# Kernel tuning notes

Measured on AMD Instinct MI355X. Metric: run time of the kernel, lower is better.

The kernel has to match this reference:

```python
import jax, jax.numpy as jnp
import numpy as np

D_MODEL = 1024
NHEAD = 16
DHEAD = D_MODEL // NHEAD
DFF = 4096
B, S = 2, 2048
R = 25                # local_attention_radius = 5*5
K = 5                 # rel_pos_max_distance
W = 2 * R + 1         # window width
EPS = 1e-5


def setup_inputs() -> dict:
    key = jax.random.key(0)
    ks = jax.random.split(key, 12)
    s = 0.02
    g = lambda k, shape: jax.random.normal(k, shape, jnp.float32) * s
    return {
        "src": jax.random.normal(ks[0], (B, S, D_MODEL), jnp.float32),
        # attention in/out projections (W stored [out,in], applied x @ W.T + b)
        "wq": g(ks[1], (D_MODEL, D_MODEL)), "bq": jnp.zeros((D_MODEL,), jnp.float32),
        "wk": g(ks[2], (D_MODEL, D_MODEL)), "bk": jnp.zeros((D_MODEL,), jnp.float32),
        "wv": g(ks[3], (D_MODEL, D_MODEL)), "bv": jnp.zeros((D_MODEL,), jnp.float32),
        "wo": g(ks[4], (D_MODEL, D_MODEL)), "bo": jnp.zeros((D_MODEL,), jnp.float32),
        # relative position embeddings, ids clipped to [-K, K] -> 2K+1 rows
        "rel_emb": g(ks[5], (2 * K + 1, DHEAD)),
        # FFN
        "w1": g(ks[6], (DFF, D_MODEL)), "b1": jnp.zeros((DFF,), jnp.float32),
        "w2": g(ks[7], (D_MODEL, DFF)), "b2": jnp.zeros((D_MODEL,), jnp.float32),
        # layernorms
        "g1": jnp.ones((D_MODEL,), jnp.float32), "beta1": jnp.zeros((D_MODEL,), jnp.float32),
        "g2": jnp.ones((D_MODEL,), jnp.float32), "beta2": jnp.zeros((D_MODEL,), jnp.float32),
    }


def _layernorm(x, g, b):
    m = x.mean(-1, keepdims=True)
    v = ((x - m) ** 2).mean(-1, keepdims=True)
    return (x - m) * jax.lax.rsqrt(v + EPS) * g + b


def _rel_window_attention(x, wq, bq, wk, bk, wv, bv, wo, bo, rel_emb):
    b, s, d = x.shape

    def proj(w, bias):
        return (x @ w.T + bias).reshape(b, s, NHEAD, DHEAD).transpose(0, 2, 1, 3)

    q = proj(wq, bq)  # [B,H,S,Dh]
    k = proj(wk, bk)
    v = proj(wv, bv)

    offsets = jnp.arange(-R, R + 1)                     # [W]
    j = jnp.arange(s)[:, None] + offsets[None, :]       # [S,W] absolute key index
    valid = (j >= 0) & (j < s)
    jc = jnp.clip(j, 0, s - 1)

    scale = 1.0 / np.sqrt(DHEAD).astype(np.float32)
    k_win = k[:, :, jc]                                 # [B,H,S,W,Dh] banded gather
    scores = jnp.einsum('bhsd,bhswd->bhsw', q, k_win) * scale
    rel_ids = jnp.clip(offsets, -K, K) + K              # [W]
    scores = scores + jnp.einsum('bhsd,wd->bhsw', q, rel_emb[rel_ids]) * scale
    scores = jnp.where(valid[None, None], scores, jnp.float32(-1e30))
    attn = jax.nn.softmax(scores, axis=-1)              # [B,H,S,W]

    v_win = v[:, :, jc]                                 # [B,H,S,W,Dh]
    out = jnp.einsum('bhsw,bhswd->bhsd', attn, v_win)
    out = out.transpose(0, 2, 1, 3).reshape(b, s, d)
    return out @ wo.T + bo


def reference(src, wq, bq, wk, bk, wv, bv, wo, bo, rel_emb,
              w1, b1, w2, b2, g1, beta1, g2, beta2):
    # post-norm (norm_first=False default) transformer block, dropout=0 (eval)
    z = _rel_window_attention(src, wq, bq, wk, bk, wv, bv, wo, bo, rel_emb)
    x = _layernorm(src + z, g1, beta1)
    ff = jax.nn.relu(x @ w1.T + b1) @ w2.T + b2
    return _layernorm(x + ff, g2, beta2)
```

## Files before the change

### kernel.cpp

```cpp
#include <hip/hip_runtime.h>


#define D_MODEL 1024
#define SEQ     2048
#define NROWS   4096
#define WIN     51
#define RAD     25

typedef __attribute__((ext_vector_type(8))) __bf16 bf16x8;
typedef __attribute__((ext_vector_type(4))) float  floatx4;

__device__ __forceinline__ unsigned short f2bf(float x) {
    unsigned u = __float_as_uint(x);
    unsigned r = u + 0x7fffu + ((u >> 16) & 1u);
    return (unsigned short)(r >> 16);
}
__device__ __forceinline__ float bf2f(unsigned short h) {
    return __uint_as_float(((unsigned)h) << 16);
}

__device__ __forceinline__ void gld16(const unsigned short* g, unsigned short* l) {
    __builtin_amdgcn_global_load_lds(
        (const __attribute__((address_space(1))) unsigned int*)g,
        (__attribute__((address_space(3))) unsigned int*)l,
        16, 0, 0);
}

__device__ __forceinline__ void cvtgrp(const float* __restrict__ in,
                                       unsigned short* __restrict__ out, int g) {
    float4 f = ((const float4*)in)[g];
    ushort4 u;
    u.x = f2bf(f.x); u.y = f2bf(f.y); u.z = f2bf(f.z); u.w = f2bf(f.w);
    ((ushort4*)out)[g] = u;
}

__global__ __launch_bounds__(256)
void cvt_all(const float* __restrict__ src,
             const float* __restrict__ wq, const float* __restrict__ wk,
             const float* __restrict__ wv, const float* __restrict__ wo,
             const float* __restrict__ w1, const float* __restrict__ w2,
             const float* __restrict__ bq, const float* __restrict__ bk,
             const float* __restrict__ bv,
             unsigned short* __restrict__ xb,
             unsigned short* __restrict__ wqkvb,
             unsigned short* __restrict__ wob,
             unsigned short* __restrict__ w1b,
             unsigned short* __restrict__ w2b,
             float* __restrict__ bqkv)
{
    int g = blockIdx.x * 256 + threadIdx.x;
    if (g >= 4194496) return;
    if (g < 1048576) { cvtgrp(src, xb, g); return; }
    g -= 1048576;
    if (g < 262144) { cvtgrp(wq, wqkvb, g); return; }
    g -= 262144;
    if (g < 262144) { cvtgrp(wk, wqkvb + 1048576, g); return; }
    g -= 262144;
    if (g < 262144) { cvtgrp(wv, wqkvb + 2097152, g); return; }
    g -= 262144;
    if (g < 262144) { cvtgrp(wo, wob, g); return; }
    g -= 262144;
    if (g < 1048576) { cvtgrp(w1, w1b, g); return; }
    g -= 1048576;
    if (g < 1048576) { cvtgrp(w2, w2b, g); return; }
    g -= 1048576;
    float4 f = (g < 64) ? ((const float4*)bq)[g]
             : (g < 128) ? ((const float4*)bk)[g - 64]
                         : ((const float4*)bv)[g - 128];
    ((float4*)bqkv)[g] = f;
}

__global__ __launch_bounds__(256, 2)
void gemm_dp(const unsigned short* __restrict__ A,
             const unsigned short* __restrict__ Wt,
             const float* __restrict__ bias,
             unsigned short* __restrict__ Cb,
             int kstride, int kloop, int T, int tncnt,
             int ldc, int relu, size_t sstep1, size_t sstep2)
{
    __shared__ __attribute__((aligned(16))) unsigned short AS[3 * 8192];
    __shared__ __attribute__((aligned(16))) unsigned short BS[3 * 4096];

    const int id = blockIdx.x;
    const int s  = id / T;
    const int t0 = id - s * T;
    const int sid = (t0 & 7) * (T >> 3) + (t0 >> 3);
    const int bm = (sid / tncnt) * 256;
    const int bn = (sid % tncnt) * 128;

    const int tid  = threadIdx.x;
    const int lane = tid & 63;
    const int wave = tid >> 6;
    const int wr   = wave >> 1;
    const int wc   = wave & 1;
    const int fm   = lane & 15;
    const int fq   = lane >> 4;

    const int kofs = s * kloop;
    const int NT   = kloop >> 5;

    const int ks  = (tid >> 3) & 7;
    const int gi  = tid ^ ks;
    const int r0s = gi >> 2;
    const int c2s = gi & 3;
    const unsigned short* Agp = A  + (size_t)(bm + r0s) * kstride + kofs + c2s * 8;
    const unsigned short* Wgp = Wt + (size_t)(bn + r0s) * kstride + kofs + c2s * 8;
    const size_t istep = (size_t)64 * kstride;

    const int rA  = wr * 128 + fm;
    const int rB  = wc * 64  + fm;
    const int c0A = ((((rA << 2) | fq) ^ (fm >> 1)) << 3);
    const int c0B = ((((rB << 2) | fq) ^ (fm >> 1)) << 3);

    {
        const unsigned short* Ap = Agp;
        const unsigned short* Wp = Wgp;
        gld16(Ap,             AS + tid * 8);
        gld16(Ap + istep,     AS + tid * 8 + 2048);
        gld16(Ap + 2 * istep, AS + tid * 8 + 4096);
        gld16(Ap + 3 * istep, AS + tid * 8 + 6144);
        gld16(Wp,             BS + tid * 8);
        gld16(Wp + istep,     BS + tid * 8 + 2048);
        Ap += 32; Wp += 32;
        gld16(Ap,             AS + 8192 + tid * 8);
        gld16(Ap + istep,     AS + 8192 + tid * 8 + 2048);
        gld16(Ap + 2 * istep, AS + 8192 + tid * 8 + 4096);
        gld16(Ap + 3 * istep, AS + 8192 + tid * 8 + 6144);
        gld16(Wp,             BS + 4096 + tid * 8);
        gld16(Wp + istep,     BS + 4096 + tid * 8 + 2048);
    }
    asm volatile("s_waitcnt vmcnt(6)" ::: "memory");
    __builtin_amdgcn_sched_barrier(0);
    __builtin_amdgcn_s_barrier();
    __builtin_amdgcn_sched_barrier(0);

    floatx4 acc[8][4] = {};
    const unsigned short* Aga = Agp + 64;
    const unsigned short* Wga = Wgp + 64;
    int cbA = 0, cbB = 0;
    int pbA = 16384, pbB = 8192;

    for (int t = 0; t < NT; t++) {
        const bool pf = (t + 2 < NT);

        bf16x8 af[8], bf[4];
        #pragma unroll
        for (int mi = 0; mi < 8; mi++)
            af[mi] = *(const bf16x8*)(AS + cbA + c0A + mi * 512);
        #pragma unroll
        for (int ni = 0; ni < 4; ni++)
            bf[ni] = *(const bf16x8*)(BS + cbB + c0B + ni * 512);

        if (pf) {
            gld16(Aga,             AS + pbA + tid * 8);
            gld16(Aga + istep,     AS + pbA + tid * 8 + 2048);
            gld16(Aga + 2 * istep, AS + pbA + tid * 8 + 4096);
            gld16(Aga + 3 * istep, AS + pbA + tid * 8 + 6144);
            gld16(Wga,             BS + pbB + tid * 8);
            gld16(Wga + istep,     BS + pbB + tid * 8 + 2048);
        }

        __builtin_amdgcn_s_setprio(1);
        #pragma unroll
        for (int mi = 0; mi < 8; mi++)
            #pragma unroll
            for (int ni = 0; ni < 4; ni++)
                acc[mi][ni] = __builtin_amdgcn_mfma_f32_16x16x32_bf16(
                    af[mi], bf[ni], acc[mi][ni], 0, 0, 0);
        __builtin_amdgcn_s_setprio(0);

        if (t + 1 < NT) {
            if (pf) asm volatile("s_waitcnt vmcnt(6)" ::: "memory");
            else    asm volatile("s_waitcnt vmcnt(0)" ::: "memory");
            __builtin_amdgcn_sched_barrier(0);
            __builtin_amdgcn_s_barrier();
            __builtin_amdgcn_sched_barrier(0);
        }
        cbA = (cbA == 16384) ? 0 : cbA + 8192;
        cbB = (cbB == 8192)  ? 0 : cbB + 4096;
        pbA = (pbA == 16384) ? 0 : pbA + 8192;
        pbB = (pbB == 8192)  ? 0 : pbB + 4096;
        Aga += 32;
        Wga += 32;
    }

    unsigned short* Co = Cb + (size_t)(s & 1) * sstep1 + (size_t)(s >> 1) * sstep2;
    const int r0  = bm + wr * 128 + fq * 4;
    const int c0e = bn + wc * 64 + fm;
    #pragma unroll
    for (int mi = 0; mi < 8; mi++) {
        #pragma unroll
        for (int ni = 0; ni < 4; ni++) {
            const int col = c0e + ni * 16;
            const float bv = bias ? bias[col] : 0.0f;
            #pragma unroll
            for (int rr = 0; rr < 4; rr++) {
                const int row = r0 + mi * 16 + rr;
                float v = acc[mi][ni][rr] + bv;
                if (relu) v = fmaxf(v, 0.0f);
                Co[(size_t)row * ldc + col] = f2bf(v);
            }
        }
    }
}

__global__ __launch_bounds__(512, 2)
void gemm8p(const unsigned short* __restrict__ A,
            const unsigned short* __restrict__ Wt,
            const float* __restrict__ bias,
            unsigned short* __restrict__ Cb,
            int kstride, int kloop, int T, int tncnt,
            int ldc, int relu, size_t sstep1, size_t sstep2)
{
    __shared__ __attribute__((aligned(16))) unsigned short AS[2 * 16384];
    __shared__ __attribute__((aligned(16))) unsigned short BS[2 * 16384];

    const int id = blockIdx.x;
    const int sl = id / T;
    const int t0 = id - sl * T;
    const int sid = (t0 & 7) * (T >> 3) + (t0 >> 3);
    const int bm = (sid / tncnt) * 256;
    const int bn = (sid % tncnt) * 256;

    const int tid  = threadIdx.x;
    const int lane = tid & 63;
    const int wave = tid >> 6;
    const int wr   = wave >> 2;
    const int wc   = wave & 3;
    const int fm   = lane & 15;
    const int fq   = lane >> 4;

    const int kofs  = sl * kloop;
    const int NITER = kloop >> 7;

    const int srow = tid >> 3;
    const int scol = ((tid & 7) ^ ((tid >> 3) & 7)) * 8;
    const unsigned short* PA = A  + (size_t)(bm + srow) * kstride + kofs + scol;
    const unsigned short* PW = Wt + (size_t)(bn + srow) * kstride + kofs + scol;
    const size_t rs64 = (size_t)64 * kstride;

    const int aoff = (wr * 128 + fm) * 64;
    const int boff = (wc * 64  + fm) * 64;
    const int ck0  = (fq ^ (fm & 7)) * 8;
    const int ck1  = ck0 ^ 32;

    floatx4 acc[8][4] = {};

    auto STG = [&](const unsigned short* g, int h, unsigned short* l) {
        gld16(g + (size_t)(2 * h)     * rs64, l + h * 8192 + tid * 8);
        gld16(g + (size_t)(2 * h + 1) * rs64, l + h * 8192 + 4096 + tid * 8);
    };
    auto rdA = [&](bf16x8 (&d)[4][2], int bufb, int mb) {
        #pragma unroll
        for (int mi = 0; mi < 4; mi++) {
            d[mi][0] = *(const bf16x8*)(AS + bufb + aoff + (mb + mi) * 1024 + ck0);
            d[mi][1] = *(const bf16x8*)(AS + bufb + aoff + (mb + mi) * 1024 + ck1);
        }
    };
    auto rdB = [&](bf16x8 (&d)[2][2], int bufb, int nb) {
        #pragma unroll
        for (int ni = 0; ni < 2; ni++) {
            d[ni][0] = *(const bf16x8*)(BS + bufb + boff + (nb + ni) * 1024 + ck0);
            d[ni][1] = *(const bf16x8*)(BS + bufb + boff + (nb + ni) * 1024 + ck1);
        }
    };
    auto mmq = [&](bf16x8 (&a)[4][2], bf16x8 (&b)[2][2], int mb, int nb) {
        __builtin_amdgcn_s_setprio(1);
        #pragma unroll
        for (int ks = 0; ks < 2; ks++)
            #pragma unroll
            for (int mi = 0; mi < 4; mi++)
                #pragma unroll
                for (int ni = 0; ni < 2; ni++)
                    acc[mb + mi][nb + ni] = __builtin_amdgcn_mfma_f32_16x16x32_bf16(
                        a[mi][ks], b[ni][ks], acc[mb + mi][nb + ni], 0, 0, 0);
        __builtin_amdgcn_s_setprio(0);
    };
    auto barpre = [&]() {
        __builtin_amdgcn_sched_barrier(0);
        __builtin_amdgcn_s_barrier();
        asm volatile("s_waitcnt lgkmcnt(0)" ::: "memory");
        __builtin_amdgcn_sched_barrier(0);
    };
    auto barpost = [&]() {
        __builtin_amdgcn_sched_barrier(0);
        __builtin_amdgcn_s_barrier();
        __builtin_amdgcn_sched_barrier(0);
    };

    unsigned short* AS0 = AS;            unsigned short* AS1 = AS + 16384;
    unsigned short* BS0 = BS;            unsigned short* BS1 = BS + 16384;

    STG(PA, 0, AS0); STG(PA, 1, AS0);
    STG(PW, 0, BS0); STG(PW, 1, BS0);
    STG(PW + 64, 0, BS1); STG(PW + 64, 1, BS1);
    __builtin_amdgcn_sched_barrier(0);
    asm volatile("s_waitcnt vmcnt(4)" ::: "memory");
    __builtin_amdgcn_sched_barrier(0);
    __builtin_amdgcn_s_barrier();
    __builtin_amdgcn_sched_barrier(0);

    for (int it = 0; it < NITER; it++) {
        const bool more = (it + 1 < NITER);
        bf16x8 a03[4][2], a47[4][2], b01[2][2], b23[2][2];

        rdA(a03, 0, 0); rdB(b01, 0, 0);
        STG(PA + 64, 0, AS1);
        barpre(); mmq(a03, b01, 0, 0); barpost();
        rdB(b23, 0, 2);
        STG(PA + 64, 1, AS1);
        barpre(); mmq(a03, b23, 0, 2); barpost();
        rdA(a47, 0, 4);
        if (more) STG(PW + 128, 0, BS0);
        barpre(); mmq(a47, b01, 4, 0); barpost();
        if (more) STG(PW + 128, 1, BS0);
        __builtin_amdgcn_sched_barrier(0);
        if (more) asm volatile("s_waitcnt vmcnt(4)" ::: "memory");
        else      asm volatile("s_waitcnt vmcnt(0)" ::: "memory");
        __builtin_amdgcn_sched_barrier(0);
        __builtin_amdgcn_s_barrier();
        __builtin_amdgcn_sched_barrier(0);
        mmq(a47, b23, 4, 2); barpost();
        rdA(a03, 16384, 0); rdB(b01, 16384, 0);
        if (more) STG(PA + 128, 0, AS0);
        barpre(); mmq(a03, b01, 0, 0); barpost();
        rdB(b23, 16384, 2);
        if (more) STG(PA + 128, 1, AS0);
        barpre(); mmq(a03, b23, 0, 2); barpost();
        rdA(a47, 16384, 4);
        if (more) STG(PW + 192, 0, BS1);
        barpre(); mmq(a47, b01, 4, 0); barpost();
        if (more) {
            STG(PW + 192, 1, BS1);
            __builtin_amdgcn_sched_barrier(0);
            asm volatile("s_waitcnt vmcnt(4)" ::: "memory");
        }
        __builtin_amdgcn_sched_barrier(0);
        __builtin_amdgcn_s_barrier();
        __builtin_amdgcn_sched_barrier(0);
        mmq(a47, b23, 4, 2); barpost();

        PA += 128; PW += 128;
    }

    unsigned short* Co = Cb + (size_t)(sl & 1) * sstep1 + (size_t)(sl >> 1) * sstep2;
    const int r0  = bm + wr * 128 + fq * 4;
    const int c0e = bn + wc * 64 + fm;
    #pragma unroll
    for (int mi = 0; mi < 8; mi++) {
        #pragma unroll
        for (int ni = 0; ni < 4; ni++) {
            const int col = c0e + ni * 16;
            const float bv = bias ? bias[col] : 0.0f;
            #pragma unroll
            for (int rr = 0; rr < 4; rr++) {
                const int row = r0 + mi * 16 + rr;
                float v = acc[mi][ni][rr] + bv;
                if (relu) v = fmaxf(v, 0.0f);
                Co[(size_t)row * ldc + col] = f2bf(v);
            }
        }
    }
}

__global__ __launch_bounds__(256, 2)
void attn_mfma(const unsigned short* __restrict__ qkv,
               const float* __restrict__ rel,
               unsigned short* __restrict__ attnb)
{
    __shared__ __attribute__((aligned(16))) unsigned short Qs[64 * 72];
    __shared__ __attribute__((aligned(16))) unsigned short Ks[128 * 72];
    __shared__ __attribute__((aligned(16))) unsigned short Vt[64 * 168];
    __shared__ __attribute__((aligned(16))) unsigned short Rs[16 * 72];
    __shared__ __attribute__((aligned(16))) unsigned short Pl[4 * 16 * 104];
    __shared__ float Qrl[4 * 16 * 12];

    const int t   = threadIdx.x;
    const int blk = blockIdx.x;
    const int st  = blk & 31;
    const int h   = (blk >> 5) & 15;
    const int b   = blk >> 9;
    const int s0  = st << 6;
    const int brow0 = b * SEQ;

    const int trow = t >> 3;
    const int tc   = (t & 7) * 8;
    const uint4 z4 = make_uint4(0, 0, 0, 0);

    #pragma unroll
    for (int p = 0; p < 2; p++) {
        int r = trow + p * 32;
        uint4 v = *(const uint4*)(qkv + (size_t)(brow0 + s0 + r) * 3072 + h * 64 + tc);
        *(uint4*)(Qs + r * 72 + tc) = v;
    }
    #pragma unroll
    for (int p = 0; p < 4; p++) {
        int kr = trow + p * 32;
        int ka = s0 - 25 + kr;
        bool in = (ka >= 0) & (ka < SEQ);
        uint4 kv = z4, vv = z4;
        if (in) {
            kv = *(const uint4*)(qkv + (size_t)(brow0 + ka) * 3072 + 1024 + h * 64 + tc);
            vv = *(const uint4*)(qkv + (size_t)(brow0 + ka) * 3072 + 2048 + h * 64 + tc);
        }
        *(uint4*)(Ks + kr * 72 + tc) = kv;
        const unsigned short* e = (const unsigned short*)&vv;
        #pragma unroll
        for (int j = 0; j < 8; j++)
            Vt[(tc + j) * 168 + kr] = e[j];
    }
    if (t < 176) {
        float4 f = ((const float4*)rel)[t];
        int fi = t * 4, rr = fi >> 6, cc = fi & 63;
        ushort4 u;
        u.x = f2bf(f.x); u.y = f2bf(f.y); u.z = f2bf(f.z); u.w = f2bf(f.w);
        *(ushort4*)(Rs + rr * 72 + cc) = u;
    } else {
        int fi = 704 + (t - 176) * 4, rr = fi >> 6, cc = fi & 63;
        *(ushort4*)(Rs + rr * 72 + cc) = make_ushort4(0, 0, 0, 0);
    }
    {
        int n = t * 4, w2 = n >> 8, rem = n & 255, rr = rem >> 4, cc = 80 + (rem & 15);
        *(ushort4*)(Pl + w2 * (16 * 104) + rr * 104 + cc) = make_ushort4(0, 0, 0, 0);
    }
    for (int idx = t; idx < 320; idx += 256) {
        int r = idx / 5, cchunk = idx % 5;
        *(uint4*)(Vt + r * 168 + 128 + cchunk * 8) = z4;
    }
    __syncthreads();

    const int wave = t >> 6;
    const int lane = t & 63;
    const int fm   = lane & 15;
    const int fk8  = (lane >> 4) * 8;
    const int S0w  = s0 + wave * 16;
    unsigned short* Plw = Pl + wave * (16 * 104);
    float* Ql = Qrl + wave * (16 * 12);

    bf16x8 qa0 = *(const bf16x8*)(Qs + (wave * 16 + fm) * 72 + fk8);
    bf16x8 qa1 = *(const bf16x8*)(Qs + (wave * 16 + fm) * 72 + fk8 + 32);

    floatx4 Sc[5];
    #pragma unroll
    for (int nt = 0; nt < 5; nt++) {
        bf16x8 kb0 = *(const bf16x8*)(Ks + (wave * 16 + nt * 16 + fm) * 72 + fk8);
        bf16x8 kb1 = *(const bf16x8*)(Ks + (wave * 16 + nt * 16 + fm) * 72 + fk8 + 32);
        floatx4 acc = {0.f, 0.f, 0.f, 0.f};
        acc = __builtin_amdgcn_mfma_f32_16x16x32_bf16(qa0, kb0, acc, 0, 0, 0);
        acc = __builtin_amdgcn_mfma_f32_16x16x32_bf16(qa1, kb1, acc, 0, 0, 0);
        Sc[nt] = acc;
    }
    {
        bf16x8 rb0 = *(const bf16x8*)(Rs + fm * 72 + fk8);
        bf16x8 rb1 = *(const bf16x8*)(Rs + fm * 72 + fk8 + 32);
        floatx4 qr = {0.f, 0.f, 0.f, 0.f};
        qr = __builtin_amdgcn_mfma_f32_16x16x32_bf16(qa0, rb0, qr, 0, 0, 0);
        qr = __builtin_amdgcn_mfma_f32_16x16x32_bf16(qa1, rb1, qr, 0, 0, 0);
        if (fm < 12) {
            #pragma unroll
            for (int reg = 0; reg < 4; reg++)
                Ql[((lane >> 4) * 4 + reg) * 12 + fm] = qr[reg];
        }
    }

    float inv[4];
    const int iq0 = (lane >> 4) * 4;
    #pragma unroll
    for (int reg = 0; reg < 4; reg++) {
        const int i = iq0 + reg;
        float sc[5];
        float mx = -1e30f;
        #pragma unroll
        for (int nt = 0; nt < 5; nt++) {
            int c   = nt * 16 + fm;
            int off = c - 25 - i;
            int ka  = S0w - 25 + c;
            bool valid = (off >= -RAD) & (off <= RAD) & (ka >= 0) & (ka < SEQ);
            int rid = min(max(off, -5), 5) + 5;
            float v = valid ? (Sc[nt][reg] + Ql[i * 12 + rid]) * 0.125f : -1e30f;
            sc[nt] = v;
            mx = fmaxf(mx, v);
        }
        #pragma unroll
        for (int o = 1; o < 16; o <<= 1) mx = fmaxf(mx, __shfl_xor(mx, o));
        float sum = 0.f;
        #pragma unroll
        for (int nt = 0; nt < 5; nt++) {
            float e = __expf(sc[nt] - mx);
            sum += e;
            Plw[i * 104 + nt * 16 + fm] = f2bf(e);
        }
        #pragma unroll
        for (int o = 1; o < 16; o <<= 1) sum += __shfl_xor(sum, o);
        inv[reg] = 1.0f / sum;
    }

    floatx4 O[4] = {};
    #pragma unroll
    for (int kc = 0; kc < 3; kc++) {
        bf16x8 pa = *(const bf16x8*)(Plw + fm * 104 + fk8 + kc * 32);
        #pragma unroll
        for (int nt = 0; nt < 4; nt++) {
            bf16x8 vb = *(const bf16x8*)(Vt + (nt * 16 + fm) * 168 + wave * 16 + fk8 + kc * 32);
            O[nt] = __builtin_amdgcn_mfma_f32_16x16x32_bf16(pa, vb, O[nt], 0, 0, 0);
        }
    }

    #pragma unroll
    for (int nt = 0; nt < 4; nt++) {
        const int d = nt * 16 + fm;
        #pragma unroll
        for (int reg = 0; reg < 4; reg++) {
            const int i = iq0 + reg;
            attnb[(size_t)(brow0 + S0w + i) * 1024 + h * 64 + d] = f2bf(O[nt][reg] * inv[reg]);
        }
    }
}

__global__ __launch_bounds__(256)
void ln_fuse(const float* __restrict__ resf,
             const unsigned short* __restrict__ resb,
             const unsigned short* __restrict__ p0,
             const unsigned short* __restrict__ p1,
             const unsigned short* __restrict__ p2,
             const unsigned short* __restrict__ p3,
             const float* __restrict__ cbias,
             const float* __restrict__ gamma,
             const float* __restrict__ beta,
             float* __restrict__ outf,
             unsigned short* __restrict__ outb)
{
    const int wave = threadIdx.x >> 6;
    const int lane = threadIdx.x & 63;
    const int row = blockIdx.x * 4 + wave;
    const size_t base = (size_t)row * D_MODEL;

    float x[16];
    float sum = 0.0f, sq = 0.0f;
    #pragma unroll
    for (int i = 0; i < 4; i++) {
        const int c4 = lane + i * 64;
        ushort4 u0 = ((const ushort4*)(p0 + base))[c4];
        ushort4 u1 = ((const ushort4*)(p1 + base))[c4];
        float4 cb = ((const float4*)cbias)[c4];
        float4 va;
        if (resf) {
            va = ((const float4*)(resf + base))[c4];
        } else {
            ushort4 ua = ((const ushort4*)(resb + base))[c4];
            va.x = bf2f(ua.x); va.y = bf2f(ua.y); va.z = bf2f(ua.z); va.w = bf2f(ua.w);
        }
        float e0 = va.x + bf2f(u0.x) + bf2f(u1.x) + cb.x;
        float e1 = va.y + bf2f(u0.y) + bf2f(u1.y) + cb.y;
        float e2 = va.z + bf2f(u0.z) + bf2f(u1.z) + cb.z;
        float e3 = va.w + bf2f(u0.w) + bf2f(u1.w) + cb.w;
        if (p2) {
            ushort4 u2 = ((const ushort4*)(p2 + base))[c4];
            ushort4 u3 = ((const ushort4*)(p3 + base))[c4];
            e0 += bf2f(u2.x) + bf2f(u3.x);
            e1 += bf2f(u2.y) + bf2f(u3.y);
            e2 += bf2f(u2.z) + bf2f(u3.z);
            e3 += bf2f(u2.w) + bf2f(u3.w);
        }
        x[i*4+0] = e0; x[i*4+1] = e1; x[i*4+2] = e2; x[i*4+3] = e3;
        sum += e0 + e1 + e2 + e3;
        sq  += e0*e0 + e1*e1 + e2*e2 + e3*e3;
    }
    #pragma unroll
    for (int off = 32; off > 0; off >>= 1) {
        sum += __shfl_xor(sum, off);
        sq  += __shfl_xor(sq,  off);
    }
    const float mean = sum * (1.0f / 1024.0f);
    const float var  = sq  * (1.0f / 1024.0f) - mean * mean;
    const float rs   = rsqrtf(var + 1e-5f);

    #pragma unroll
    for (int i = 0; i < 4; i++) {
        const int c4 = lane + i * 64;
        float4 g4 = ((const float4*)gamma)[c4];
        float4 b4 = ((const float4*)beta)[c4];
        float4 o;
        o.x = (x[i*4+0] - mean) * rs * g4.x + b4.x;
        o.y = (x[i*4+1] - mean) * rs * g4.y + b4.y;
        o.z = (x[i*4+2] - mean) * rs * g4.z + b4.z;
        o.w = (x[i*4+3] - mean) * rs * g4.w + b4.w;
        if (outf) ((float4*)(outf + base))[c4] = o;
        if (outb) {
            ushort4 u;
            u.x = f2bf(o.x); u.y = f2bf(o.y); u.z = f2bf(o.z); u.w = f2bf(o.w);
            ((ushort4*)(outb + base))[c4] = u;
        }
    }
}

extern "C" void kernel_launch(void* const* d_in, const int* in_sizes, int n_in,
                              void* d_out, int out_size, void* d_ws, size_t ws_size,
                              hipStream_t stream)
{
    const float* src = (const float*)d_in[0];
    const float* wq  = (const float*)d_in[1];
    const float* bq  = (const float*)d_in[2];
    const float* wk  = (const float*)d_in[3];
    const float* bk  = (const float*)d_in[4];
    const float* wv  = (const float*)d_in[5];
    const float* bv  = (const float*)d_in[6];
    const float* wo  = (const float*)d_in[7];
    const float* bo  = (const float*)d_in[8];
    const float* rel = (const float*)d_in[9];
    const float* w1  = (const float*)d_in[10];
    const float* b1  = (const float*)d_in[11];
    const float* w2  = (const float*)d_in[12];
    const float* b2  = (const float*)d_in[13];
    const float* g1  = (const float*)d_in[14];
    const float* be1 = (const float*)d_in[15];
    const float* g2  = (const float*)d_in[16];
    const float* be2 = (const float*)d_in[17];
    float* out = (float*)d_out;

    char* ws = (char*)d_ws;
    const size_t MB = 1048576;
    unsigned short* wqkvb = (unsigned short*)(ws + 0);
    unsigned short* wob   = (unsigned short*)(ws + 6  * MB);
    unsigned short* w1b   = (unsigned short*)(ws + 8  * MB);
    unsigned short* w2b   = (unsigned short*)(ws + 16 * MB);
    float*          bqkv  = (float*)         (ws + 24 * MB);
    unsigned short* xb    = (unsigned short*)(ws + 25 * MB);
    unsigned short* attnb = xb;
    unsigned short* qkvb  = (unsigned short*)(ws + 33 * MB);
    unsigned short* z01   = (unsigned short*)(ws + 33 * MB);
    unsigned short* x1b   = (unsigned short*)(ws + 49 * MB);
    unsigned short* ff1b  = (unsigned short*)(ws + 57 * MB);
    unsigned short* f01   = (unsigned short*)(ws + 0);
    const size_t SL    = (size_t)NROWS * 1024;
    const size_t SOFF2 = (size_t)12 * MB;

    const dim3 blk(256);
    const dim3 blk5(512);
    cvt_all<<<16385, blk, 0, stream>>>(src, wq, wk, wv, wo, w1, w2, bq, bk, bv,
                                       xb, wqkvb, wob, w1b, w2b, bqkv);
    gemm_dp<<<384, blk, 0, stream>>>(xb, wqkvb, bqkv, qkvb, 1024, 1024, 384, 24,
                                     3072, 0, 0, 0);
    attn_mfma<<<1024, blk, 0, stream>>>(qkvb, rel, attnb);
    gemm8p<<<256, blk5, 0, stream>>>(attnb, wob, nullptr, z01, 1024, 256, 64, 4,
                                     1024, 0, SL, SOFF2);
    ln_fuse<<<NROWS / 4, blk, 0, stream>>>(src, nullptr, z01, z01 + SL,
                                           z01 + SOFF2, z01 + SOFF2 + SL,
                                           bo, g1, be1, nullptr, x1b);
    gemm8p<<<256, blk5, 0, stream>>>(x1b, w1b, b1, ff1b, 1024, 1024, 256, 16,
                                     4096, 1, 0, 0);
    gemm8p<<<256, blk5, 0, stream>>>(ff1b, w2b, nullptr, f01, 4096, 1024, 64, 4,
                                     1024, 0, SL, SOFF2);
    ln_fuse<<<NROWS / 4, blk, 0, stream>>>(nullptr, x1b, f01, f01 + SL,
                                           f01 + SOFF2, f01 + SOFF2 + SL,
                                           b2, g2, be2, out, nullptr);
}
```

Baseline: 305.8 us.

## Overlap wo/w1/w2 weight conversion with QKV GEMM in one launch

Splits the single conversion kernel so only the input and QKV weights are converted before the QKV projection. The remaining wo, w1 and w2 conversion runs as extra blocks of the QKV GEMM launch, so that memory-bound conversion can overlap the GEMM's 384 compute blocks. The GEMM also gets its strides, loop count and tile mapping fixed as compile-time constants. The cost is a larger grid with mixed block types whose scheduling is left to hardware.

```diff
diff --git a/kernel.cpp b/kernel.cpp
--- a/kernel.cpp
+++ b/kernel.cpp
@@ -35,21 +35,17 @@
 }
 
 __global__ __launch_bounds__(256)
-void cvt_all(const float* __restrict__ src,
-             const float* __restrict__ wq, const float* __restrict__ wk,
-             const float* __restrict__ wv, const float* __restrict__ wo,
-             const float* __restrict__ w1, const float* __restrict__ w2,
-             const float* __restrict__ bq, const float* __restrict__ bk,
-             const float* __restrict__ bv,
-             unsigned short* __restrict__ xb,
-             unsigned short* __restrict__ wqkvb,
-             unsigned short* __restrict__ wob,
-             unsigned short* __restrict__ w1b,
-             unsigned short* __restrict__ w2b,
-             float* __restrict__ bqkv)
+void cvt1(const float* __restrict__ src,
+          const float* __restrict__ wq, const float* __restrict__ wk,
+          const float* __restrict__ wv,
+          const float* __restrict__ bq, const float* __restrict__ bk,
+          const float* __restrict__ bv,
+          unsigned short* __restrict__ xb,
+          unsigned short* __restrict__ wqkvb,
+          float* __restrict__ bqkv)
 {
     int g = blockIdx.x * 256 + threadIdx.x;
-    if (g >= 4194496) return;
+    if (g >= 1835200) return;
     if (g < 1048576) { cvtgrp(src, xb, g); return; }
     g -= 1048576;
     if (g < 262144) { cvtgrp(wq, wqkvb, g); return; }
@@ -58,12 +54,6 @@
     g -= 262144;
     if (g < 262144) { cvtgrp(wv, wqkvb + 2097152, g); return; }
     g -= 262144;
-    if (g < 262144) { cvtgrp(wo, wob, g); return; }
-    g -= 262144;
-    if (g < 1048576) { cvtgrp(w1, w1b, g); return; }
-    g -= 1048576;
-    if (g < 1048576) { cvtgrp(w2, w2b, g); return; }
-    g -= 1048576;
     float4 f = (g < 64) ? ((const float4*)bq)[g]
              : (g < 128) ? ((const float4*)bk)[g - 64]
                          : ((const float4*)bv)[g - 128];
@@ -71,22 +61,33 @@
 }
 
 __global__ __launch_bounds__(256, 2)
-void gemm_dp(const unsigned short* __restrict__ A,
+void qkv_cvt(const unsigned short* __restrict__ A,
              const unsigned short* __restrict__ Wt,
              const float* __restrict__ bias,
              unsigned short* __restrict__ Cb,
-             int kstride, int kloop, int T, int tncnt,
-             int ldc, int relu, size_t sstep1, size_t sstep2)
+             const float* __restrict__ wo, const float* __restrict__ w1,
+             const float* __restrict__ w2,
+             unsigned short* __restrict__ wob,
+             unsigned short* __restrict__ w1b,
+             unsigned short* __restrict__ w2b)
 {
     __shared__ __attribute__((aligned(16))) unsigned short AS[3 * 8192];
     __shared__ __attribute__((aligned(16))) unsigned short BS[3 * 4096];
 
-    const int id = blockIdx.x;
-    const int s  = id / T;
-    const int t0 = id - s * T;
-    const int sid = (t0 & 7) * (T >> 3) + (t0 >> 3);
-    const int bm = (sid / tncnt) * 256;
-    const int bn = (sid % tncnt) * 128;
+    if (blockIdx.x >= 384) {
+        int g = (blockIdx.x - 384) * 256 + threadIdx.x;
+        if (g < 262144) { cvtgrp(wo, wob, g); return; }
+        g -= 262144;
+        if (g < 1048576) { cvtgrp(w1, w1b, g); return; }
+        g -= 1048576;
+        cvtgrp(w2, w2b, g);
+        return;
+    }
+
+    const int t0 = blockIdx.x;
+    const int sid = (t0 & 7) * 48 + (t0 >> 3);
+    const int bm = (sid / 24) * 256;
+    const int bn = (sid % 24) * 128;
 
     const int tid  = threadIdx.x;
     const int lane = tid & 63;
@@ -96,16 +97,15 @@
     const int fm   = lane & 15;
     const int fq   = lane >> 4;
 
-    const int kofs = s * kloop;
-    const int NT   = kloop >> 5;
+    const int NT = 32;
 
     const int ks  = (tid >> 3) & 7;
     const int gi  = tid ^ ks;
     const int r0s = gi >> 2;
     const int c2s = gi & 3;
-    const unsigned short* Agp = A  + (size_t)(bm + r0s) * kstride + kofs + c2s * 8;
-    const unsigned short* Wgp = Wt + (size_t)(bn + r0s) * kstride + kofs + c2s * 8;
-    const size_t istep = (size_t)64 * kstride;
+    const unsigned short* Agp = A  + (size_t)(bm + r0s) * 1024 + c2s * 8;
+    const unsigned short* Wgp = Wt + (size_t)(bn + r0s) * 1024 + c2s * 8;
+    const size_t istep = (size_t)64 * 1024;
 
     const int rA  = wr * 128 + fm;
     const int rB  = wc * 64  + fm;
@@ -184,7 +184,6 @@
         Wga += 32;
     }
 
-    unsigned short* Co = Cb + (size_t)(s & 1) * sstep1 + (size_t)(s >> 1) * sstep2;
     const int r0  = bm + wr * 128 + fq * 4;
     const int c0e = bn + wc * 64 + fm;
     #pragma unroll
@@ -192,13 +191,13 @@
         #pragma unroll
         for (int ni = 0; ni < 4; ni++) {
             const int col = c0e + ni * 16;
-            const float bv = bias ? bias[col] : 0.0f;
+            const float bv = bias[col];
             #pragma unroll
             for (int rr = 0; rr < 4; rr++) {
                 const int row = r0 + mi * 16 + rr;
+                Co_store: ;
                 float v = acc[mi][ni][rr] + bv;
-                if (relu) v = fmaxf(v, 0.0f);
-                Co[(size_t)row * ldc + col] = f2bf(v);
+                Cb[(size_t)row * 3072 + col] = f2bf(v);
             }
         }
     }
@@ -637,10 +636,9 @@
 
     const dim3 blk(256);
     const dim3 blk5(512);
-    cvt_all<<<16385, blk, 0, stream>>>(src, wq, wk, wv, wo, w1, w2, bq, bk, bv,
-                                       xb, wqkvb, wob, w1b, w2b, bqkv);
-    gemm_dp<<<384, blk, 0, stream>>>(xb, wqkvb, bqkv, qkvb, 1024, 1024, 384, 24,
-                                     3072, 0, 0, 0);
+    cvt1<<<7169, blk, 0, stream>>>(src, wq, wk, wv, bq, bk, bv, xb, wqkvb, bqkv);
+    qkv_cvt<<<9600, blk, 0, stream>>>(xb, wqkvb, bqkv, qkvb,
+                                      wo, w1, w2, wob, w1b, w2b);
     attn_mfma<<<1024, blk, 0, stream>>>(qkvb, rel, attnb);
     gemm8p<<<256, blk5, 0, stream>>>(attnb, wob, nullptr, z01, 1024, 256, 64, 4,
                                      1024, 0, SL, SOFF2);
```

Result: faster. 297.4 us (-2.8%).
